# Performance work log

Hardware: AMD Instinct MI355X
Metric: run time of the kernel (lower is better)

Reference implementation:

```python
import jax, jax.numpy as jnp
import numpy as np

B, D, H, E, TOPK = 65536, 1024, 512, 8, 2
LN_EPS = 1e-5
LB_WEIGHT = 0.01


def setup_inputs() -> dict:
    key = jax.random.key(0)
    ks = jax.random.split(key, 5)
    x = jax.random.normal(ks[0], (B, D), dtype=jnp.float32)
    W1 = jax.random.normal(ks[1], (D, H), dtype=jnp.float32) * 0.02
    b1 = jnp.zeros((H,), dtype=jnp.float32)
    ln_w = jnp.ones((H,), dtype=jnp.float32)
    ln_b = jnp.zeros((H,), dtype=jnp.float32)
    W2 = jax.random.normal(ks[2], (H, E), dtype=jnp.float32) * 0.02
    b2 = jnp.zeros((E,), dtype=jnp.float32)
    return {"x": x, "W1": W1, "b1": b1, "ln_w": ln_w, "ln_b": ln_b, "W2": W2, "b2": b2}


def _gate_logits(x, W1, b1, ln_w, ln_b, W2, b2):
    h = x @ W1 + b1                     # [B, H]
    mu = jnp.mean(h, axis=-1, keepdims=True)
    var = jnp.mean(jnp.square(h - mu), axis=-1, keepdims=True)
    h = (h - mu) * jax.lax.rsqrt(var + LN_EPS) * ln_w + ln_b
    h = jax.nn.gelu(h, approximate=False)  # torch nn.GELU default = exact erf
    return h @ W2 + b2                  # [B, E]


def reference(x, W1, b1, ln_w, ln_b, W2, b2):
    logits = _gate_logits(x, W1, b1, ln_w, ln_b, W2, b2)
    # sparse top-K routing (eval mode: no exploration noise)
    vals, idx = jax.lax.top_k(logits, TOPK)           # [B, K]
    rows = jnp.arange(logits.shape[0])[:, None]
    sparse = jnp.full_like(logits, -jnp.inf).at[rows, idx].set(vals)
    weights = jax.nn.softmax(sparse, axis=-1)         # zeros off top-k
    # Switch-style load-balance loss
    f = (weights > 0).astype(weights.dtype).mean(axis=0)  # fraction routed per expert
    P = weights.mean(axis=0)                              # mean gate prob per expert
    lb_loss = LB_WEIGHT * (E * jnp.sum(f * P))
    return weights, lb_loss
```

## Files before the change

### kernel.cpp

```cpp
#include <hip/hip_runtime.h>
#include <cstdint>
#include <cstddef>


typedef _Float16 f16;
typedef _Float16 f16x8 __attribute__((ext_vector_type(8)));
typedef float f32x4 __attribute__((ext_vector_type(4)));

#define B_ROWS 65536
#define D_DIM 1024
#define H_DIM 512
#define E_DIM 8
#define BM 64
#define BK 32
#define THREADS 512
#define NSUPER 16
#define LDPX 72
#define SLABH 4608
#define BUFH 9216
#define IMG_CH (H_DIM * BK)
#define IMG_TOTAL (32 * IMG_CH)
#define GACC_OFF ((size_t)2 * IMG_TOTAL * sizeof(f16))

__global__ void prep_split(const float* __restrict__ W1,
                           f16* __restrict__ wh, f16* __restrict__ wl) {
  int id = blockIdx.x * 256 + threadIdx.x;
  int h = id & (H_DIM - 1);
  int kg = id >> 9;
  int c = kg >> 2;
  int kk0 = (kg & 3) * 8;
  int k0 = kg * 8;
  f16x8 hv, lv;
#pragma unroll
  for (int j = 0; j < 8; ++j) {
    float v = W1[(size_t)(k0 + j) * H_DIM + h] * 64.0f;
    f16 hi = (f16)v;
    hv[j] = hi;
    lv[j] = (f16)((v - (float)hi) * 256.0f);
  }
  size_t o = (size_t)c * IMG_CH + (size_t)h * BK + kk0;
  *(f16x8*)&wh[o] = hv;
  *(f16x8*)&wl[o] = lv;
}

__global__ void zero_acc(float* __restrict__ acc) {
  if (threadIdx.x < 16) acc[threadIdx.x] = 0.0f;
}

__global__ __launch_bounds__(THREADS, 4) void fused_main(
    const float* __restrict__ x,
    const f16* __restrict__ wh, const f16* __restrict__ wl,
    const float* __restrict__ b1, const float* __restrict__ lnw,
    const float* __restrict__ lnb, const float* __restrict__ W2,
    const float* __restrict__ b2, float* __restrict__ out,
    float* __restrict__ gacc) {
  __shared__ __align__(16) char pool[45632];
  f16* sx = (f16*)pool;

  const int tid = threadIdx.x;
  const int lane = tid & 63;
  const int wv = tid >> 6;
  const int l15 = lane & 15;
  const int l4 = lane >> 4;
  const int64_t row0 = (int64_t)blockIdx.x * BM;

  const int srow = tid >> 3;
  const int sk = (tid & 7) * 8;
  const int swo = srow * LDPX + sk;
  const float* xbase = x + (row0 + srow) * D_DIM + sk;

  const f16* whp = wh + (wv * 64 + l15) * BK + l4 * 8;

  f32x4 acc[4][4];
#pragma unroll
  for (int m = 0; m < 4; ++m)
#pragma unroll
    for (int n = 0; n < 4; ++n) acc[m][n] = (f32x4){0.f, 0.f, 0.f, 0.f};

  f16x8 setB[2][4];

#define ISSUE(si, C, half)                                                    \
  do {                                                                        \
    const f16* p = whp + (size_t)((C) & 31) * IMG_CH + (half) * 1024;         \
    setB[si][0] = *(const f16x8*)(p);                                         \
    setB[si][1] = *(const f16x8*)(p + 512);                                   \
    setB[si][2] = *(const f16x8*)(p + IMG_TOTAL);                             \
    setB[si][3] = *(const f16x8*)(p + IMG_TOTAL + 512);                       \
  } while (0)

#define CHUNK_HALF(si, nh, ch, bufv)                                          \
  do {                                                                        \
    __builtin_amdgcn_s_setprio(1);                                            \
    _Pragma("unroll") for (int m = 0; m < 4; ++m) {                           \
      const int ao = (bufv)*BUFH + (m * 16 + l15) * LDPX + (ch)*32 + l4 * 8;  \
      f16x8 ah = *(const f16x8*)&sx[ao];                                      \
      f16x8 al = *(const f16x8*)&sx[ao + SLABH];                              \
      f16x8 ahs;                                                              \
      _Pragma("unroll") for (int q = 0; q < 8; ++q) ahs[q] =                  \
          ah[q] * (f16)0.00390625f;                                           \
      acc[m][(nh)*2 + 0] = __builtin_amdgcn_mfma_f32_16x16x32_f16(            \
          ah, setB[si][0], acc[m][(nh)*2 + 0], 0, 0, 0);                      \
      acc[m][(nh)*2 + 1] = __builtin_amdgcn_mfma_f32_16x16x32_f16(            \
          ah, setB[si][1], acc[m][(nh)*2 + 1], 0, 0, 0);                      \
      acc[m][(nh)*2 + 0] = __builtin_amdgcn_mfma_f32_16x16x32_f16(            \
          al, setB[si][0], acc[m][(nh)*2 + 0], 0, 0, 0);                      \
      acc[m][(nh)*2 + 1] = __builtin_amdgcn_mfma_f32_16x16x32_f16(            \
          al, setB[si][1], acc[m][(nh)*2 + 1], 0, 0, 0);                      \
      acc[m][(nh)*2 + 0] = __builtin_amdgcn_mfma_f32_16x16x32_f16(            \
          ahs, setB[si][2], acc[m][(nh)*2 + 0], 0, 0, 0);                     \
      acc[m][(nh)*2 + 1] = __builtin_amdgcn_mfma_f32_16x16x32_f16(            \
          ahs, setB[si][3], acc[m][(nh)*2 + 1], 0, 0, 0);                     \
    }                                                                         \
    __builtin_amdgcn_s_setprio(0);                                            \
  } while (0)

#define WRITE_SLAB(bufv)                                                      \
  do {                                                                        \
    float vv[8] = {xv0.x, xv0.y, xv0.z, xv0.w, xv1.x, xv1.y, xv1.z, xv1.w};   \
    f16x8 hv, lv;                                                             \
    _Pragma("unroll") for (int q = 0; q < 8; ++q) {                           \
      float t = vv[q] * 64.0f;                                                \
      f16 hh = (f16)t;                                                        \
      hv[q] = hh;                                                             \
      lv[q] = (f16)(t - (float)hh);                                           \
    }                                                                         \
    *(f16x8*)&sx[(bufv)*BUFH + swo] = hv;                                     \
    *(f16x8*)&sx[(bufv)*BUFH + SLABH + swo] = lv;                             \
  } while (0)

#define SLAB_BARRIER()                                                        \
  do {                                                                        \
    asm volatile("s_waitcnt lgkmcnt(0)" ::: "memory");                        \
    __builtin_amdgcn_s_barrier();                                             \
    __builtin_amdgcn_sched_barrier(0);                                        \
  } while (0)

  float4 xv0 = *(const float4*)(xbase);
  float4 xv1 = *(const float4*)(xbase + 4);
  WRITE_SLAB(0);
  ISSUE(0, 0, 0);
  ISSUE(1, 0, 1);
  xv0 = *(const float4*)(xbase + 64);
  xv1 = *(const float4*)(xbase + 68);
  SLAB_BARRIER();

  for (int s = 0; s < NSUPER; ++s) {
    const int buf = s & 1;
    CHUNK_HALF(0, 0, 0, buf);
    ISSUE(0, 2 * s + 1, 0);
    CHUNK_HALF(1, 1, 0, buf);
    ISSUE(1, 2 * s + 1, 1);
    CHUNK_HALF(0, 0, 1, buf);
    ISSUE(0, 2 * s + 2, 0);
    CHUNK_HALF(1, 1, 1, buf);
    ISSUE(1, 2 * s + 2, 1);
    WRITE_SLAB(buf ^ 1);
    xv0 = *(const float4*)(xbase + (((s + 2) & 15) * 64));
    xv1 = *(const float4*)(xbase + (((s + 2) & 15) * 64) + 4);
    SLAB_BARRIER();
  }
#undef ISSUE
#undef CHUNK_HALF
#undef WRITE_SLAB
#undef SLAB_BARRIER
  __syncthreads();

  float* eW2T = (float*)pool;
  float* eStat = (float*)(pool + 24576);
  float* eLog = (float*)(pool + 28672);
  float* eMu = (float*)(pool + 45056);
  float* eRs = (float*)(pool + 45312);
  float* eFP = (float*)(pool + 45568);

  {
    float4 wa = *(const float4*)&W2[tid * 8];
    float4 wb = *(const float4*)&W2[tid * 8 + 4];
    *(float4*)&eW2T[tid * 12] = wa;
    *(float4*)&eW2T[tid * 12 + 4] = wb;
  }
  if (tid < 16) eFP[tid] = 0.0f;

  float bb[4], lw[4], lb[4];
#pragma unroll
  for (int n = 0; n < 4; ++n) {
    int col = wv * 64 + n * 16 + l15;
    bb[n] = b1[col] * 4096.0f;
    lw[n] = lnw[col];
    lb[n] = lnb[col];
#pragma unroll
    for (int m = 0; m < 4; ++m)
#pragma unroll
      for (int r = 0; r < 4; ++r) acc[m][n][r] += bb[n];
  }

#pragma unroll
  for (int m = 0; m < 4; ++m) {
    float s1[4] = {0, 0, 0, 0};
    float s2[4] = {0, 0, 0, 0};
#pragma unroll
    for (int n = 0; n < 4; ++n)
#pragma unroll
      for (int r = 0; r < 4; ++r) {
        float vv = acc[m][n][r];
        s1[r] += vv;
        s2[r] = fmaf(vv, vv, s2[r]);
      }
#pragma unroll
    for (int d = 1; d < 16; d <<= 1)
#pragma unroll
      for (int r = 0; r < 4; ++r) {
        s1[r] += __shfl_xor(s1[r], d);
        s2[r] += __shfl_xor(s2[r], d);
      }
    if (l15 == 0) {
      int rb = m * 16 + l4 * 4;
#pragma unroll
      for (int r = 0; r < 4; ++r) {
        eStat[(wv * 64 + rb + r) * 2 + 0] = s1[r];
        eStat[(wv * 64 + rb + r) * 2 + 1] = s2[r];
      }
    }
  }
  __syncthreads();
  if (tid < BM) {
    float s1 = 0.0f, s2 = 0.0f;
#pragma unroll
    for (int w = 0; w < 8; ++w) {
      s1 += eStat[(w * 64 + tid) * 2 + 0];
      s2 += eStat[(w * 64 + tid) * 2 + 1];
    }
    float mu = s1 * (1.0f / 512.0f);
    float var = s2 * (1.0f / 512.0f) - mu * mu;
    eMu[tid] = mu;
    eRs[tid] = 1.0f / sqrtf(var + (1e-5f * 4096.0f * 4096.0f));
  }
  __syncthreads();

#pragma unroll
  for (int m = 0; m < 4; ++m) {
    int rb = m * 16 + l4 * 4;
#pragma unroll
    for (int r = 0; r < 4; ++r) {
      float mu_r = eMu[rb + r];
      float rs_r = eRs[rb + r];
      float lg[8];
#pragma unroll
      for (int e = 0; e < 8; ++e) lg[e] = 0.0f;
#pragma unroll
      for (int n = 0; n < 4; ++n) {
        int col = wv * 64 + n * 16 + l15;
        float hn = (acc[m][n][r] - mu_r) * rs_r;
        float y = fmaf(hn, lw[n], lb[n]);
        float g = 0.5f * y * (1.0f + erff(y * 0.70710678118654752440f));
        float4 w0 = *(const float4*)&eW2T[col * 12];
        float4 w1 = *(const float4*)&eW2T[col * 12 + 4];
        lg[0] = fmaf(g, w0.x, lg[0]);
        lg[1] = fmaf(g, w0.y, lg[1]);
        lg[2] = fmaf(g, w0.z, lg[2]);
        lg[3] = fmaf(g, w0.w, lg[3]);
        lg[4] = fmaf(g, w1.x, lg[4]);
        lg[5] = fmaf(g, w1.y, lg[5]);
        lg[6] = fmaf(g, w1.z, lg[6]);
        lg[7] = fmaf(g, w1.w, lg[7]);
      }
#pragma unroll
      for (int d = 1; d < 16; d <<= 1)
#pragma unroll
        for (int e = 0; e < 8; ++e) lg[e] += __shfl_xor(lg[e], d);
      if (l15 == 0) {
#pragma unroll
        for (int e = 0; e < 8; ++e) eLog[(wv * 64 + rb + r) * 8 + e] = lg[e];
      }
    }
  }
  __syncthreads();

  if (tid < BM) {
    float v[8];
#pragma unroll
    for (int e = 0; e < 8; ++e) {
      float s = b2[e];
#pragma unroll
      for (int w = 0; w < 8; ++w) s += eLog[(w * 64 + tid) * 8 + e];
      v[e] = s;
    }
    float m1 = v[0];
    int i1 = 0;
#pragma unroll
    for (int e = 1; e < 8; ++e)
      if (v[e] > m1) { m1 = v[e]; i1 = e; }
    float m2 = -3.0e38f;
    int i2 = -1;
#pragma unroll
    for (int e = 0; e < 8; ++e)
      if (e != i1 && v[e] > m2) { m2 = v[e]; i2 = e; }
    float dd = expf(m2 - m1);
    float inv = 1.0f / (1.0f + dd);
    float wA = inv, wB = dd * inv;
    float o[8];
#pragma unroll
    for (int e = 0; e < 8; ++e)
      o[e] = (e == i1) ? wA : ((e == i2) ? wB : 0.0f);
    float4* op = (float4*)&out[(row0 + tid) * 8];
    op[0] = (float4){o[0], o[1], o[2], o[3]};
    op[1] = (float4){o[4], o[5], o[6], o[7]};
    atomicAdd(&eFP[i1], 1.0f);
    atomicAdd(&eFP[i2], 1.0f);
    atomicAdd(&eFP[8 + i1], wA);
    atomicAdd(&eFP[8 + i2], wB);
  }
  __syncthreads();
  if (tid < 16) atomicAdd(&gacc[tid], eFP[tid]);
}

__global__ void lb_final(const float* __restrict__ gacc, float* __restrict__ out) {
  if (threadIdx.x == 0) {
    const float invB = 1.0f / 65536.0f;
    float s = 0.0f;
#pragma unroll
    for (int e = 0; e < 8; ++e) s += (gacc[e] * invB) * (gacc[8 + e] * invB);
    out[(size_t)B_ROWS * E_DIM] = 0.01f * 8.0f * s;
  }
}

extern "C" void kernel_launch(void* const* d_in, const int* in_sizes, int n_in,
                              void* d_out, int out_size, void* d_ws, size_t ws_size,
                              hipStream_t stream) {
  (void)in_sizes; (void)n_in; (void)out_size; (void)ws_size;
  const float* x = (const float*)d_in[0];
  const float* W1 = (const float*)d_in[1];
  const float* b1 = (const float*)d_in[2];
  const float* lnw = (const float*)d_in[3];
  const float* lnb = (const float*)d_in[4];
  const float* W2 = (const float*)d_in[5];
  const float* b2 = (const float*)d_in[6];
  float* out = (float*)d_out;
  f16* wh = (f16*)d_ws;
  f16* wl = wh + IMG_TOTAL;
  float* gacc = (float*)((char*)d_ws + GACC_OFF);

  zero_acc<<<1, 64, 0, stream>>>(gacc);
  prep_split<<<(D_DIM * H_DIM / 8) / 256, 256, 0, stream>>>(W1, wh, wl);
  fused_main<<<B_ROWS / BM, THREADS, 0, stream>>>(x, wh, wl, b1, lnw, lnb, W2, b2,
                                                  out, gacc);
  lb_final<<<1, 64, 0, stream>>>(gacc, out);
}
```

Baseline: 248.9 us.

## Stagger odd waves' chunk and m-tile order, write next slab before MFMAs

Odd waves now process the two K-chunks of each super-step in reverse order and walk the m sub-tiles in a rotated order. The aim is to spread LDS bank and L2 pressure across waves instead of having all waves hit the same addresses at once. The next x slab is now written to LDS at the start of each iteration rather than after the MFMAs, and the last iterations skip the wrap-around prefetch. This adds branch divergence between waves and a different prefetch sequence for the odd path, which must stay correct at the chunk boundaries.

```diff
diff --git a/kernel.cpp b/kernel.cpp
--- a/kernel.cpp
+++ b/kernel.cpp
@@ -88,29 +88,35 @@
     setB[si][3] = *(const f16x8*)(p + IMG_TOTAL + 512);                       \
   } while (0)
 
-#define CHUNK_HALF(si, nh, ch, bufv)                                          \
+#define CH_M(si, nh, ch, bufv, MM)                                            \
+  do {                                                                        \
+    const int ao = (bufv)*BUFH + ((MM)*16 + l15) * LDPX + (ch)*32 + l4 * 8;   \
+    f16x8 ah = *(const f16x8*)&sx[ao];                                        \
+    f16x8 al = *(const f16x8*)&sx[ao + SLABH];                                \
+    f16x8 ahs;                                                                \
+    _Pragma("unroll") for (int q = 0; q < 8; ++q) ahs[q] =                    \
+        ah[q] * (f16)0.00390625f;                                             \
+    acc[MM][(nh)*2 + 0] = __builtin_amdgcn_mfma_f32_16x16x32_f16(             \
+        ah, setB[si][0], acc[MM][(nh)*2 + 0], 0, 0, 0);                       \
+    acc[MM][(nh)*2 + 1] = __builtin_amdgcn_mfma_f32_16x16x32_f16(             \
+        ah, setB[si][1], acc[MM][(nh)*2 + 1], 0, 0, 0);                       \
+    acc[MM][(nh)*2 + 0] = __builtin_amdgcn_mfma_f32_16x16x32_f16(             \
+        al, setB[si][0], acc[MM][(nh)*2 + 0], 0, 0, 0);                       \
+    acc[MM][(nh)*2 + 1] = __builtin_amdgcn_mfma_f32_16x16x32_f16(             \
+        al, setB[si][1], acc[MM][(nh)*2 + 1], 0, 0, 0);                       \
+    acc[MM][(nh)*2 + 0] = __builtin_amdgcn_mfma_f32_16x16x32_f16(             \
+        ahs, setB[si][2], acc[MM][(nh)*2 + 0], 0, 0, 0);                      \
+    acc[MM][(nh)*2 + 1] = __builtin_amdgcn_mfma_f32_16x16x32_f16(             \
+        ahs, setB[si][3], acc[MM][(nh)*2 + 1], 0, 0, 0);                      \
+  } while (0)
+
+#define CHUNK_HALF(si, nh, ch, bufv, MA, MB, MC, MD)                          \
   do {                                                                        \
     __builtin_amdgcn_s_setprio(1);                                            \
-    _Pragma("unroll") for (int m = 0; m < 4; ++m) {                           \
-      const int ao = (bufv)*BUFH + (m * 16 + l15) * LDPX + (ch)*32 + l4 * 8;  \
-      f16x8 ah = *(const f16x8*)&sx[ao];                                      \
-      f16x8 al = *(const f16x8*)&sx[ao + SLABH];                              \
-      f16x8 ahs;                                                              \
-      _Pragma("unroll") for (int q = 0; q < 8; ++q) ahs[q] =                  \
-          ah[q] * (f16)0.00390625f;                                           \
-      acc[m][(nh)*2 + 0] = __builtin_amdgcn_mfma_f32_16x16x32_f16(            \
-          ah, setB[si][0], acc[m][(nh)*2 + 0], 0, 0, 0);                      \
-      acc[m][(nh)*2 + 1] = __builtin_amdgcn_mfma_f32_16x16x32_f16(            \
-          ah, setB[si][1], acc[m][(nh)*2 + 1], 0, 0, 0);                      \
-      acc[m][(nh)*2 + 0] = __builtin_amdgcn_mfma_f32_16x16x32_f16(            \
-          al, setB[si][0], acc[m][(nh)*2 + 0], 0, 0, 0);                      \
-      acc[m][(nh)*2 + 1] = __builtin_amdgcn_mfma_f32_16x16x32_f16(            \
-          al, setB[si][1], acc[m][(nh)*2 + 1], 0, 0, 0);                      \
-      acc[m][(nh)*2 + 0] = __builtin_amdgcn_mfma_f32_16x16x32_f16(            \
-          ahs, setB[si][2], acc[m][(nh)*2 + 0], 0, 0, 0);                     \
-      acc[m][(nh)*2 + 1] = __builtin_amdgcn_mfma_f32_16x16x32_f16(            \
-          ahs, setB[si][3], acc[m][(nh)*2 + 1], 0, 0, 0);                     \
-    }                                                                         \
+    CH_M(si, nh, ch, bufv, MA);                                               \
+    CH_M(si, nh, ch, bufv, MB);                                               \
+    CH_M(si, nh, ch, bufv, MC);                                               \
+    CH_M(si, nh, ch, bufv, MD);                                               \
     __builtin_amdgcn_s_setprio(0);                                            \
   } while (0)
 
@@ -135,31 +141,52 @@
     __builtin_amdgcn_sched_barrier(0);                                        \
   } while (0)
 
+  const bool oddw = (wv & 1) != 0;
+
   float4 xv0 = *(const float4*)(xbase);
   float4 xv1 = *(const float4*)(xbase + 4);
   WRITE_SLAB(0);
-  ISSUE(0, 0, 0);
-  ISSUE(1, 0, 1);
+  if (!oddw) {
+    ISSUE(0, 0, 0);
+    ISSUE(1, 0, 1);
+  } else {
+    ISSUE(0, 1, 0);
+    ISSUE(1, 1, 1);
+  }
   xv0 = *(const float4*)(xbase + 64);
   xv1 = *(const float4*)(xbase + 68);
   SLAB_BARRIER();
 
   for (int s = 0; s < NSUPER; ++s) {
     const int buf = s & 1;
-    CHUNK_HALF(0, 0, 0, buf);
-    ISSUE(0, 2 * s + 1, 0);
-    CHUNK_HALF(1, 1, 0, buf);
-    ISSUE(1, 2 * s + 1, 1);
-    CHUNK_HALF(0, 0, 1, buf);
-    ISSUE(0, 2 * s + 2, 0);
-    CHUNK_HALF(1, 1, 1, buf);
-    ISSUE(1, 2 * s + 2, 1);
-    WRITE_SLAB(buf ^ 1);
-    xv0 = *(const float4*)(xbase + (((s + 2) & 15) * 64));
-    xv1 = *(const float4*)(xbase + (((s + 2) & 15) * 64) + 4);
+    if (s < NSUPER - 1) WRITE_SLAB(buf ^ 1);
+    if (s < NSUPER - 2) {
+      xv0 = *(const float4*)(xbase + (s + 2) * 64);
+      xv1 = *(const float4*)(xbase + (s + 2) * 64 + 4);
+    }
+    if (!oddw) {
+      CHUNK_HALF(0, 0, 0, buf, 0, 1, 2, 3);
+      ISSUE(0, 2 * s + 1, 0);
+      CHUNK_HALF(1, 1, 0, buf, 0, 1, 2, 3);
+      ISSUE(1, 2 * s + 1, 1);
+      CHUNK_HALF(0, 0, 1, buf, 0, 1, 2, 3);
+      ISSUE(0, 2 * s + 2, 0);
+      CHUNK_HALF(1, 1, 1, buf, 0, 1, 2, 3);
+      ISSUE(1, 2 * s + 2, 1);
+    } else {
+      CHUNK_HALF(0, 0, 1, buf, 2, 3, 0, 1);
+      ISSUE(0, 2 * s, 0);
+      CHUNK_HALF(1, 1, 1, buf, 2, 3, 0, 1);
+      ISSUE(1, 2 * s, 1);
+      CHUNK_HALF(0, 0, 0, buf, 2, 3, 0, 1);
+      ISSUE(0, 2 * s + 3, 0);
+      CHUNK_HALF(1, 1, 0, buf, 2, 3, 0, 1);
+      ISSUE(1, 2 * s + 3, 1);
+    }
     SLAB_BARRIER();
   }
 #undef ISSUE
+#undef CH_M
 #undef CHUNK_HALF
 #undef WRITE_SLAB
 #undef SLAB_BARRIER
```

New measurement: 271.9 us. 1.09x slower.
